# Optimization experiments

Hardware: AMD Instinct MI355X
Metric: run time of the kernel (lower is better)

The kernel has to match this reference:

```python
import jax, jax.numpy as jnp
import numpy as np

N, D, E = 100000, 128, 800000

def setup_inputs() -> dict:
    key = jax.random.key(0)
    k1, k2, k3, k4 = jax.random.split(key, 4)
    z = jax.random.normal(k1, (N, D), dtype=jnp.float32)
    edge_index = jax.random.randint(k2, (2, E), 0, N, dtype=jnp.int64)
    # PyTorch-style init scale for Linear layers (kaiming-uniform-ish via normal is fine for a numeric reference)
    W1 = jax.random.normal(k3, (2 * D, D), dtype=jnp.float32) * (1.0 / np.sqrt(2 * D))
    b1 = jnp.zeros((D,), dtype=jnp.float32)
    W2 = jax.random.normal(k4, (D, 1), dtype=jnp.float32) * (1.0 / np.sqrt(D))
    b2 = jnp.zeros((1,), dtype=jnp.float32)
    return {"z": z, "edge_index": edge_index, "W1": W1, "b1": b1, "W2": W2, "b2": b2}

def reference(z, edge_index, W1, b1, W2, b2):
    # row/col gather of node embeddings
    row, col = edge_index[0], edge_index[1]
    # cat([z[row], z[col]]) @ W1 == z[row] @ W1[:D] + z[col] @ W1[D:]
    # -> avoids materializing the [E, 2D] concatenated tensor
    d = z.shape[1]
    h = z[row] @ W1[:d] + z[col] @ W1[d:] + b1          # [E, D]
    h = jax.nn.relu(h)                                   # Dropout(0.1) is identity in eval mode
    out = h @ W2 + b2                                    # [E, 1]
    return out.squeeze(-1)                               # [E]
```

## Files before the change

kernel.cpp:

```cpp
#include <hip/hip_runtime.h>

#define DDIM 128

typedef __bf16 bf16x8 __attribute__((ext_vector_type(8)));
typedef float  floatx4 __attribute__((ext_vector_type(4)));

__global__ __launch_bounds__(256, 4) void precompute_uv_mfma_q8(
    const float* __restrict__ z, const float* __restrict__ W1,
    const float* __restrict__ b1,
    unsigned char* __restrict__ U8, unsigned char* __restrict__ V8,
    float* __restrict__ u_scale, float* __restrict__ v_scale,
    int N, int nchunks)
{
    __shared__ unsigned short WsF[32 * 64 * 8];

    const int t    = threadIdx.x;
    const int lane = t & 63;
    const int w    = t >> 6;
    const int half = blockIdx.x;
    unsigned char* __restrict__ dst8 = half ? V8 : U8;
    float*         __restrict__ dscl = half ? v_scale : u_scale;
    const float*   __restrict__ Wh   = W1 + (size_t)half * DDIM * DDIM;

    const int mrow = lane & 15;
    const int quad = lane >> 4;
    const int gy   = gridDim.y;

    float4 rx[8];
    auto issue_loads = [&](int ch) {
        int grow = ch * 64 + w * 16 + mrow;
        if (grow > N - 1) grow = N - 1;
        const float* zrow = z + (size_t)grow * DDIM;
        #pragma unroll
        for (int ks = 0; ks < 4; ++ks) {
            const int k0 = ks * 32 + quad * 8;
            rx[2 * ks]     = *(const float4*)(zrow + k0);
            rx[2 * ks + 1] = *(const float4*)(zrow + k0 + 4);
        }
    };

    if (blockIdx.y < nchunks) issue_loads(blockIdx.y);

    {
        const int nlow = lane & 15;
        const int kq   = (lane >> 4) & 3;
        #pragma unroll
        for (int i = 0; i < 8; ++i) {
            const int ntks = w + i * 4;
            const int nt = ntks >> 2, ks = ntks & 3;
            const int n  = nt * 16 + nlow;
            const int kb = ks * 32 + kq * 8;
            float f[8];
            #pragma unroll
            for (int j = 0; j < 8; ++j)
                f[j] = Wh[(kb + j) * DDIM + n];
            unsigned pk[4];
            #pragma unroll
            for (int j = 0; j < 4; ++j)
                asm("v_cvt_pk_bf16_f32 %0, %1, %2"
                    : "=v"(pk[j]) : "v"(f[2 * j]), "v"(f[2 * j + 1]));
            *(uint4*)&WsF[(ntks * 64 + lane) * 8] = *(const uint4*)pk;
        }
    }

    float bval[8];
    #pragma unroll
    for (int nt = 0; nt < 8; ++nt)
        bval[nt] = (half == 0) ? b1[nt * 16 + mrow] : 0.f;

    __syncthreads();

    for (int chunk = blockIdx.y; chunk < nchunks; chunk += gy) {
        bf16x8 afrag[4];
        #pragma unroll
        for (int ks = 0; ks < 4; ++ks) {
            const float4 x0 = rx[2 * ks];
            const float4 x1 = rx[2 * ks + 1];
            unsigned pk[4];
            asm("v_cvt_pk_bf16_f32 %0, %1, %2" : "=v"(pk[0]) : "v"(x0.x), "v"(x0.y));
            asm("v_cvt_pk_bf16_f32 %0, %1, %2" : "=v"(pk[1]) : "v"(x0.z), "v"(x0.w));
            asm("v_cvt_pk_bf16_f32 %0, %1, %2" : "=v"(pk[2]) : "v"(x1.x), "v"(x1.y));
            asm("v_cvt_pk_bf16_f32 %0, %1, %2" : "=v"(pk[3]) : "v"(x1.z), "v"(x1.w));
            afrag[ks] = __builtin_bit_cast(bf16x8, *(const uint4*)pk);
        }

        const int nxt = chunk + gy;
        if (nxt < nchunks) issue_loads(nxt);

        floatx4 acc[8];
        #pragma unroll
        for (int nt = 0; nt < 8; ++nt)
            acc[nt] = (floatx4){bval[nt], bval[nt], bval[nt], bval[nt]};

        #pragma unroll
        for (int ks = 0; ks < 4; ++ks) {
            #pragma unroll
            for (int nt = 0; nt < 8; ++nt) {
                const bf16x8 b = __builtin_bit_cast(bf16x8,
                    *(const uint4*)&WsF[((nt * 4 + ks) * 64 + lane) * 8]);
                acc[nt] = __builtin_amdgcn_mfma_f32_16x16x32_bf16(afrag[ks], b, acc[nt], 0, 0, 0);
            }
        }

        #pragma unroll
        for (int r = 0; r < 4; ++r) {
            float mx = fmaxf(fmaxf(fabsf(acc[0][r]), fabsf(acc[1][r])),
                             fabsf(acc[2][r]));
            mx = fmaxf(fmaxf(mx, fabsf(acc[3][r])), fabsf(acc[4][r]));
            mx = fmaxf(fmaxf(mx, fabsf(acc[5][r])), fabsf(acc[6][r]));
            mx = fmaxf(mx, fabsf(acc[7][r]));
            #pragma unroll
            for (int m = 1; m < 16; m <<= 1)
                mx = fmaxf(mx, __shfl_xor(mx, m, 16));
            mx = fmaxf(mx, 1e-20f);
            const float inv = 127.f * __builtin_amdgcn_rcpf(mx);

            unsigned char bytes[8];
            #pragma unroll
            for (int nt = 0; nt < 8; ++nt) {
                const float fq = fmaf(acc[nt][r], inv, 12583040.0f);
                bytes[nt] = (unsigned char)(__builtin_bit_cast(unsigned, fq) & 0xffu);
            }
            const int grow = chunk * 64 + w * 16 + quad * 4 + r;
            if (grow < N) {
                *(uint2*)&dst8[(size_t)grow * DDIM + mrow * 8] =
                    *(const uint2*)bytes;
                if (mrow == 0) dscl[grow] = mx * (1.f / 127.f);
            }
        }
    }
}

__global__ __launch_bounds__(256) void edge_kernel_i8(
    const int* __restrict__ ei,
    const unsigned char* __restrict__ U8, const unsigned char* __restrict__ V8,
    const float* __restrict__ u_scale, const float* __restrict__ v_scale,
    const float* __restrict__ W2, const float* __restrict__ b2,
    float* __restrict__ out, int E)
{
    const int t  = threadIdx.x;
    const int q  = t & 7;
    const int g0 = (blockIdx.x * 32 + (t >> 3)) * 4;
    if (g0 >= E) return;

    float ww[16];
    #pragma unroll
    for (int k = 0; k < 16; ++k)
        ww[k] = W2[(k & 7) * 16 + 2 * q + (k >> 3)];

    int rows[4], cols[4];
    if (g0 + 3 < E) {
        const int4 r4 = *(const int4*)(ei + g0);
        const int4 c4 = *(const int4*)(ei + (size_t)E + g0);
        rows[0]=r4.x; rows[1]=r4.y; rows[2]=r4.z; rows[3]=r4.w;
        cols[0]=c4.x; cols[1]=c4.y; cols[2]=c4.z; cols[3]=c4.w;
    } else {
        #pragma unroll
        for (int i = 0; i < 4; ++i) {
            const int gi = (g0 + i < E) ? (g0 + i) : (E - 1);
            rows[i] = ei[gi];
            cols[i] = ei[(size_t)E + gi];
        }
    }

    uint4 uu[4], vv[4];
    #pragma unroll
    for (int i = 0; i < 4; ++i)
        uu[i] = *(const uint4*)(U8 + (size_t)rows[i] * DDIM + q * 16);
    #pragma unroll
    for (int i = 0; i < 4; ++i)
        vv[i] = *(const uint4*)(V8 + (size_t)cols[i] * DDIM + q * 16);

    float su[4], sv[4];
    #pragma unroll
    for (int i = 0; i < 4; ++i) { su[i] = u_scale[rows[i]]; sv[i] = v_scale[cols[i]]; }

    const float bias = b2[0];

    float sres[4];
    #pragma unroll
    for (int i = 0; i < 4; ++i) {
        const unsigned uw0 = uu[i].x, uw1 = uu[i].y, uw2 = uu[i].z, uw3 = uu[i].w;
        const unsigned vw0 = vv[i].x, vw1 = vv[i].y, vw2 = vv[i].z, vw3 = vv[i].w;
        const float c = -128.f * (su[i] + sv[i]);
        float s = 0.f;
        #pragma unroll
        for (int k = 0; k < 16; ++k) {
            const unsigned uwk = (k < 4) ? uw0 : (k < 8) ? uw1 : (k < 12) ? uw2 : uw3;
            const unsigned vwk = (k < 4) ? vw0 : (k < 8) ? vw1 : (k < 12) ? vw2 : vw3;
            const float uf = (float)((uwk >> (8 * (k & 3))) & 0xffu);
            const float vf = (float)((vwk >> (8 * (k & 3))) & 0xffu);
            const float h  = fmaf(su[i], uf, fmaf(sv[i], vf, c));
            s = fmaf(fmaxf(h, 0.f), ww[k], s);
        }
        s += __shfl_down(s, 4, 8);
        s += __shfl_down(s, 2, 8);
        s += __shfl_down(s, 1, 8);
        sres[i] = s + bias;
    }

    if (q == 0) {
        if (g0 + 3 < E) {
            float4 o; o.x = sres[0]; o.y = sres[1]; o.z = sres[2]; o.w = sres[3];
            *(float4*)&out[g0] = o;
        } else {
            #pragma unroll
            for (int i = 0; i < 4; ++i)
                if (g0 + i < E) out[g0 + i] = sres[i];
        }
    }
}

__global__ __launch_bounds__(256) void edge_fused_fallback(
    const float* __restrict__ z, const int* __restrict__ ei,
    const float* __restrict__ W1, const float* __restrict__ b1,
    const float* __restrict__ W2, const float* __restrict__ b2,
    float* __restrict__ out, int N, int E)
{
    const int tid  = blockIdx.x * 256 + threadIdx.x;
    const int e    = tid >> 6;
    const int lane = tid & 63;
    if (e >= E) return;

    const int row = ei[e];
    const int col = ei[(size_t)E + e];
    const float* zr = z + (size_t)row * DDIM;
    const float* zc = z + (size_t)col * DDIM;

    float h0 = b1[lane];
    float h1 = b1[lane + 64];
    for (int k = 0; k < DDIM; ++k) {
        const float a = zr[k];
        const float b = zc[k];
        h0 = fmaf(a, W1[k * DDIM + lane],               h0);
        h0 = fmaf(b, W1[(DDIM + k) * DDIM + lane],      h0);
        h1 = fmaf(a, W1[k * DDIM + lane + 64],          h1);
        h1 = fmaf(b, W1[(DDIM + k) * DDIM + lane + 64], h1);
    }
    float s = fmaxf(h0, 0.f) * W2[lane] + fmaxf(h1, 0.f) * W2[lane + 64];
    #pragma unroll
    for (int off = 32; off > 0; off >>= 1)
        s += __shfl_down(s, off, 64);
    if (lane == 0) out[e] = s + b2[0];
}

extern "C" void kernel_launch(void* const* d_in, const int* in_sizes, int n_in,
                              void* d_out, int out_size, void* d_ws, size_t ws_size,
                              hipStream_t stream)
{
    const float* z  = (const float*)d_in[0];
    const int*   ei = (const int*)d_in[1];
    const float* W1 = (const float*)d_in[2];
    const float* b1 = (const float*)d_in[3];
    const float* W2 = (const float*)d_in[4];
    const float* b2 = (const float*)d_in[5];
    float*       out = (float*)d_out;

    const int N = in_sizes[0] / DDIM;
    const int E = in_sizes[1] / 2;

    const size_t n128 = (size_t)N * DDIM;
    const size_t need = 2 * n128 + 2 * (size_t)N * sizeof(float) + 256;
    if (ws_size >= need) {
        unsigned char* U8 = (unsigned char*)d_ws;
        unsigned char* V8 = U8 + n128;
        float* usc = (float*)(((size_t)(V8 + n128) + 255) & ~(size_t)255);
        float* vsc = usc + N;
        const int nchunks = (N + 63) / 64;
        const int gy = nchunks < 512 ? nchunks : 512;
        hipLaunchKernelGGL(precompute_uv_mfma_q8, dim3(2, gy), dim3(256), 0, stream,
                           z, W1, b1, U8, V8, usc, vsc, N, nchunks);
        hipLaunchKernelGGL(edge_kernel_i8, dim3((E + 127) / 128), dim3(256), 0, stream,
                           ei, U8, V8, usc, vsc, W2, b2, out, E);
    } else {
        hipLaunchKernelGGL(edge_fused_fallback, dim3((E + 3) / 4), dim3(256), 0, stream,
                           z, ei, W1, b1, W2, b2, out, N, E);
    }
}
```

Before: 138.6 us.

## Compute U and V in one block and double-buffer z via global-to-LDS loads

The precompute kernel now gives each block both halves of W1 in LDS, so every z chunk is read from global memory once and produces both the U and V quantized outputs. Previously two separate block columns each read z. The z tiles are staged asynchronously into LDS with global_load_lds in a ping-pong buffer, replacing the register prefetch, and the grid shrinks to a 1D launch of up to 256 blocks. The trade-off is a large LDS footprint of roughly 128KB per block, which allows only one block per CU, plus more serial work per block. Latency hiding therefore relies on the async double buffering.

Measured after the change: 144.5 us. 4.3% more time.

```diff
diff --git a/kernel.cpp b/kernel.cpp
--- a/kernel.cpp
+++ b/kernel.cpp
@@ -5,77 +5,56 @@
 typedef __bf16 bf16x8 __attribute__((ext_vector_type(8)));
 typedef float  floatx4 __attribute__((ext_vector_type(4)));
 
-__global__ __launch_bounds__(256, 4) void precompute_uv_mfma_q8(
+#define GLOAD_LDS16(gp, lp)                                                    \
+    __builtin_amdgcn_global_load_lds(                                          \
+        (const __attribute__((address_space(1))) unsigned*)(gp),               \
+        (__attribute__((address_space(3))) unsigned*)(lp), 16, 0, 0)
+
+using Abuf = float[4][4][2][64][4];
+
+__global__ __launch_bounds__(256) void precompute_uv_mfma_q8(
     const float* __restrict__ z, const float* __restrict__ W1,
     const float* __restrict__ b1,
     unsigned char* __restrict__ U8, unsigned char* __restrict__ V8,
     float* __restrict__ u_scale, float* __restrict__ v_scale,
     int N, int nchunks)
 {
-    __shared__ unsigned short WsF[32 * 64 * 8];
+    __shared__ unsigned short WsF[2 * 32 * 64 * 8];
+    __shared__ Abuf Az0;
+    __shared__ Abuf Az1;
 
     const int t    = threadIdx.x;
     const int lane = t & 63;
     const int w    = t >> 6;
-    const int half = blockIdx.x;
-    unsigned char* __restrict__ dst8 = half ? V8 : U8;
-    float*         __restrict__ dscl = half ? v_scale : u_scale;
-    const float*   __restrict__ Wh   = W1 + (size_t)half * DDIM * DDIM;
-
     const int mrow = lane & 15;
     const int quad = lane >> 4;
-    const int gy   = gridDim.y;
-
-    float4 rx[8];
-    auto issue_loads = [&](int ch) {
+    const int gy   = gridDim.x;
+
+    auto stage = [&](int ch, Abuf& A) {
         int grow = ch * 64 + w * 16 + mrow;
         if (grow > N - 1) grow = N - 1;
-        const float* zrow = z + (size_t)grow * DDIM;
+        const float* zr = z + (size_t)grow * DDIM;
         #pragma unroll
         for (int ks = 0; ks < 4; ++ks) {
-            const int k0 = ks * 32 + quad * 8;
-            rx[2 * ks]     = *(const float4*)(zrow + k0);
-            rx[2 * ks + 1] = *(const float4*)(zrow + k0 + 4);
+            #pragma unroll
+            for (int h = 0; h < 2; ++h) {
+                const float* gp = zr + ks * 32 + quad * 8 + h * 4;
+                GLOAD_LDS16(gp, &A[w][ks][h][0][0]);
+            }
         }
     };
 
-    if (blockIdx.y < nchunks) issue_loads(blockIdx.y);
-
-    {
-        const int nlow = lane & 15;
-        const int kq   = (lane >> 4) & 3;
-        #pragma unroll
-        for (int i = 0; i < 8; ++i) {
-            const int ntks = w + i * 4;
-            const int nt = ntks >> 2, ks = ntks & 3;
-            const int n  = nt * 16 + nlow;
-            const int kb = ks * 32 + kq * 8;
-            float f[8];
-            #pragma unroll
-            for (int j = 0; j < 8; ++j)
-                f[j] = Wh[(kb + j) * DDIM + n];
-            unsigned pk[4];
-            #pragma unroll
-            for (int j = 0; j < 4; ++j)
-                asm("v_cvt_pk_bf16_f32 %0, %1, %2"
-                    : "=v"(pk[j]) : "v"(f[2 * j]), "v"(f[2 * j + 1]));
-            *(uint4*)&WsF[(ntks * 64 + lane) * 8] = *(const uint4*)pk;
-        }
-    }
-
     float bval[8];
     #pragma unroll
     for (int nt = 0; nt < 8; ++nt)
-        bval[nt] = (half == 0) ? b1[nt * 16 + mrow] : 0.f;
-
-    __syncthreads();
-
-    for (int chunk = blockIdx.y; chunk < nchunks; chunk += gy) {
+        bval[nt] = b1[nt * 16 + mrow];
+
+    auto compute = [&](int c, const Abuf& A) {
         bf16x8 afrag[4];
         #pragma unroll
         for (int ks = 0; ks < 4; ++ks) {
-            const float4 x0 = rx[2 * ks];
-            const float4 x1 = rx[2 * ks + 1];
+            const float4 x0 = *(const float4*)&A[w][ks][0][lane][0];
+            const float4 x1 = *(const float4*)&A[w][ks][1][lane][0];
             unsigned pk[4];
             asm("v_cvt_pk_bf16_f32 %0, %1, %2" : "=v"(pk[0]) : "v"(x0.x), "v"(x0.y));
             asm("v_cvt_pk_bf16_f32 %0, %1, %2" : "=v"(pk[1]) : "v"(x0.z), "v"(x0.w));
@@ -84,50 +63,105 @@
             afrag[ks] = __builtin_bit_cast(bf16x8, *(const uint4*)pk);
         }
 
-        const int nxt = chunk + gy;
-        if (nxt < nchunks) issue_loads(nxt);
-
-        floatx4 acc[8];
-        #pragma unroll
-        for (int nt = 0; nt < 8; ++nt)
-            acc[nt] = (floatx4){bval[nt], bval[nt], bval[nt], bval[nt]};
-
-        #pragma unroll
-        for (int ks = 0; ks < 4; ++ks) {
+        #pragma unroll
+        for (int h = 0; h < 2; ++h) {
+            unsigned char* __restrict__ dst8 = h ? V8 : U8;
+            float*         __restrict__ dscl = h ? v_scale : u_scale;
+
+            floatx4 acc[8];
             #pragma unroll
             for (int nt = 0; nt < 8; ++nt) {
-                const bf16x8 b = __builtin_bit_cast(bf16x8,
-                    *(const uint4*)&WsF[((nt * 4 + ks) * 64 + lane) * 8]);
-                acc[nt] = __builtin_amdgcn_mfma_f32_16x16x32_bf16(afrag[ks], b, acc[nt], 0, 0, 0);
+                const float b0 = h ? 0.f : bval[nt];
+                acc[nt] = (floatx4){b0, b0, b0, b0};
             }
-        }
-
-        #pragma unroll
-        for (int r = 0; r < 4; ++r) {
-            float mx = fmaxf(fmaxf(fabsf(acc[0][r]), fabsf(acc[1][r])),
-                             fabsf(acc[2][r]));
-            mx = fmaxf(fmaxf(mx, fabsf(acc[3][r])), fabsf(acc[4][r]));
-            mx = fmaxf(fmaxf(mx, fabsf(acc[5][r])), fabsf(acc[6][r]));
-            mx = fmaxf(mx, fabsf(acc[7][r]));
-            #pragma unroll
-            for (int m = 1; m < 16; m <<= 1)
-                mx = fmaxf(mx, __shfl_xor(mx, m, 16));
-            mx = fmaxf(mx, 1e-20f);
-            const float inv = 127.f * __builtin_amdgcn_rcpf(mx);
-
-            unsigned char bytes[8];
-            #pragma unroll
-            for (int nt = 0; nt < 8; ++nt) {
-                const float fq = fmaf(acc[nt][r], inv, 12583040.0f);
-                bytes[nt] = (unsigned char)(__builtin_bit_cast(unsigned, fq) & 0xffu);
+
+            #pragma unroll
+            for (int ks = 0; ks < 4; ++ks) {
+                #pragma unroll
+                for (int nt = 0; nt < 8; ++nt) {
+                    const bf16x8 b = __builtin_bit_cast(bf16x8,
+                        *(const uint4*)&WsF[((h * 32 + nt * 4 + ks) * 64 + lane) * 8]);
+                    acc[nt] = __builtin_amdgcn_mfma_f32_16x16x32_bf16(
+                        afrag[ks], b, acc[nt], 0, 0, 0);
+                }
             }
-            const int grow = chunk * 64 + w * 16 + quad * 4 + r;
-            if (grow < N) {
-                *(uint2*)&dst8[(size_t)grow * DDIM + mrow * 8] =
-                    *(const uint2*)bytes;
-                if (mrow == 0) dscl[grow] = mx * (1.f / 127.f);
+
+            #pragma unroll
+            for (int r = 0; r < 4; ++r) {
+                float mx = fmaxf(fmaxf(fabsf(acc[0][r]), fabsf(acc[1][r])),
+                                 fabsf(acc[2][r]));
+                mx = fmaxf(fmaxf(mx, fabsf(acc[3][r])), fabsf(acc[4][r]));
+                mx = fmaxf(fmaxf(mx, fabsf(acc[5][r])), fabsf(acc[6][r]));
+                mx = fmaxf(mx, fabsf(acc[7][r]));
+                #pragma unroll
+                for (int m = 1; m < 16; m <<= 1)
+                    mx = fmaxf(mx, __shfl_xor(mx, m, 16));
+                mx = fmaxf(mx, 1e-20f);
+                const float inv = 127.f * __builtin_amdgcn_rcpf(mx);
+
+                unsigned char bytes[8];
+                #pragma unroll
+                for (int nt = 0; nt < 8; ++nt) {
+                    const float fq = fmaf(acc[nt][r], inv, 12583040.0f);
+                    bytes[nt] = (unsigned char)(__builtin_bit_cast(unsigned, fq) & 0xffu);
+                }
+                const int grow = c * 64 + w * 16 + quad * 4 + r;
+                if (grow < N) {
+                    *(uint2*)&dst8[(size_t)grow * DDIM + mrow * 8] =
+                        *(const uint2*)bytes;
+                    if (mrow == 0) dscl[grow] = mx * (1.f / 127.f);
+                }
             }
         }
+    };
+
+    const int c0 = blockIdx.x;
+    stage(c0, Az0);
+
+    {
+        const int nlow = lane & 15;
+        const int kq   = (lane >> 4) & 3;
+        #pragma unroll 4
+        for (int i = 0; i < 16; ++i) {
+            const int s    = w + i * 4;
+            const int half = s >> 5;
+            const int ntks = s & 31;
+            const int nt = ntks >> 2, ks = ntks & 3;
+            const int n  = nt * 16 + nlow;
+            const int kb = ks * 32 + kq * 8;
+            const float* __restrict__ Wh = W1 + (size_t)half * DDIM * DDIM;
+            float f[8];
+            #pragma unroll
+            for (int j = 0; j < 8; ++j)
+                f[j] = Wh[(kb + j) * DDIM + n];
+            unsigned pk[4];
+            #pragma unroll
+            for (int j = 0; j < 4; ++j)
+                asm("v_cvt_pk_bf16_f32 %0, %1, %2"
+                    : "=v"(pk[j]) : "v"(f[2 * j]), "v"(f[2 * j + 1]));
+            *(uint4*)&WsF[(s * 64 + lane) * 8] = *(const uint4*)pk;
+        }
+    }
+
+    __syncthreads();
+
+    int c = c0;
+    while (c < nchunks) {
+        {
+            const int nx = c + gy;
+            if (nx < nchunks) stage(nx, Az1);
+            compute(c, Az0);
+            __builtin_amdgcn_s_waitcnt(0);
+        }
+        c += gy;
+        if (c >= nchunks) break;
+        {
+            const int nx = c + gy;
+            if (nx < nchunks) stage(nx, Az0);
+            compute(c, Az1);
+            __builtin_amdgcn_s_waitcnt(0);
+        }
+        c += gy;
     }
 }
 
@@ -267,8 +301,8 @@
         float* usc = (float*)(((size_t)(V8 + n128) + 255) & ~(size_t)255);
         float* vsc = usc + N;
         const int nchunks = (N + 63) / 64;
-        const int gy = nchunks < 512 ? nchunks : 512;
-        hipLaunchKernelGGL(precompute_uv_mfma_q8, dim3(2, gy), dim3(256), 0, stream,
+        const int gy = nchunks < 256 ? nchunks : 256;
+        hipLaunchKernelGGL(precompute_uv_mfma_q8, dim3(gy), dim3(256), 0, stream,
                            z, W1, b1, U8, V8, usc, vsc, N, nchunks);
         hipLaunchKernelGGL(edge_kernel_i8, dim3((E + 127) / 128), dim3(256), 0, stream,
                            ei, U8, V8, usc, vsc, W2, b2, out, E);
```
